# Optimization experiments

Measured on AMD Instinct MI355X. Metric: run time of the kernel, lower is better.

## Reference

```python
import jax, jax.numpy as jnp
import numpy as np

# NF4 codebook (bitsandbytes create_normal_map, quant_type='nf4')
NF4_CODE = jnp.array([
    -1.0, -0.6961928009986877, -0.5250730514526367, -0.39491748809814453,
    -0.28444138169288635, -0.18477343022823334, -0.09105003625154495, 0.0,
    0.07958029955625534, 0.16093020141124725, 0.24611230194568634,
    0.33791524171829224, 0.44070982933044434, 0.5626170039176941,
    0.7229568362236023, 1.0], dtype=jnp.float32)

BLOCKSIZE = 64  # bitsandbytes default
IN_F = 64
OUT_F = 64
N_TOKENS = 1048576


def _quantize_nf4(w_flat):
    # w_flat: [n_blocks, BLOCKSIZE] -> (codes int32, absmax float32)
    absmax = jnp.max(jnp.abs(w_flat), axis=1)  # [n_blocks]
    norm = w_flat / jnp.maximum(absmax, 1e-12)[:, None]
    # nearest NF4 codebook entry
    codes = jnp.argmin(jnp.abs(norm[:, :, None] - NF4_CODE[None, None, :]), axis=-1)
    return codes.astype(jnp.int32), absmax.astype(jnp.float32)


def setup_inputs() -> dict:
    key = jax.random.key(0)
    kx, kw, ka = jax.random.split(key, 3)
    x = jax.random.normal(kx, (N_TOKENS, IN_F), dtype=jnp.float32)
    # frozen base weight, quantized to NF4 blockwise (row-major [out, in] flattened)
    w_base = jax.random.normal(kw, (OUT_F, IN_F), dtype=jnp.float32) * 0.05
    n_blocks = (OUT_F * IN_F) // BLOCKSIZE
    codes, absmax = _quantize_nf4(w_base.reshape(n_blocks, BLOCKSIZE))
    adapter_w = jax.random.normal(ka, (OUT_F, IN_F), dtype=jnp.float32) * 0.05
    return {"x": x, "codes": codes, "absmax": absmax, "adapter_w": adapter_w}


def reference(x, codes, absmax, adapter_w):
    # Blockwise NF4 dequantization of the frozen base weight
    w_base = (NF4_CODE[codes] * absmax[:, None]).reshape(OUT_F, IN_F)  # [out, in]
    # y = x @ W_base^T + x @ A^T  (base(x) + adapter(x))
    return x @ w_base.T + x @ adapter_w.T
```

## Files before the change

kernel.cpp:

```cpp
#include <hip/hip_runtime.h>
#include <hip/hip_bf16.h>


#define N_TOKENS 1048576
#define WROW 36

typedef __attribute__((ext_vector_type(8))) short bf16x8;
typedef __attribute__((ext_vector_type(4))) float f32x4;

__device__ __constant__ float NF4_CODE_D[16] = {
    -1.0f, -0.6961928009986877f, -0.5250730514526367f, -0.39491748809814453f,
    -0.28444138169288635f, -0.18477343022823334f, -0.09105003625154495f, 0.0f,
    0.07958029955625534f, 0.16093020141124725f, 0.24611230194568634f,
    0.33791524171829224f, 0.44070982933044434f, 0.5626170039176941f,
    0.7229568362236023f, 1.0f};

__device__ __forceinline__ unsigned int cvt2(float lo, float hi) {
    __hip_bfloat162 h = __float22bfloat162_rn(make_float2(lo, hi));
    union { __hip_bfloat162 h; unsigned int u; } c; c.h = h;
    return c.u;
}

union BF8 { bf16x8 v; unsigned int u[4]; };

__device__ __forceinline__ void strip_compute(
    f32x4 a0, f32x4 a1, f32x4 a2, f32x4 a3,
    const unsigned int* __restrict__ wbase, float* __restrict__ yp) {
    BF8 b0, b1;
    b0.u[0] = cvt2(a0[0], a0[1]); b0.u[1] = cvt2(a0[2], a0[3]);
    b0.u[2] = cvt2(a1[0], a1[1]); b0.u[3] = cvt2(a1[2], a1[3]);
    b1.u[0] = cvt2(a2[0], a2[1]); b1.u[1] = cvt2(a2[2], a2[3]);
    b1.u[2] = cvt2(a3[0], a3[1]); b1.u[3] = cvt2(a3[2], a3[3]);
#pragma unroll
    for (int j = 0; j < 4; ++j) {
        bf16x8 w0 = *(const bf16x8*)(wbase + j * 16 * WROW);
        bf16x8 w1 = *(const bf16x8*)(wbase + j * 16 * WROW + 16);
        f32x4 c = {0.f, 0.f, 0.f, 0.f};
        c = __builtin_amdgcn_mfma_f32_16x16x32_bf16(w0, b0.v, c, 0, 0, 0);
        c = __builtin_amdgcn_mfma_f32_16x16x32_bf16(w1, b1.v, c, 0, 0, 0);
        __builtin_nontemporal_store(c, (f32x4*)(yp + j * 16));
    }
}

__global__ __launch_bounds__(256) void qlora_fused_kernel(
    const float* __restrict__ x,
    const int* __restrict__ codes,
    const float* __restrict__ absmax,
    const float* __restrict__ adapter,
    float* __restrict__ y) {

    __shared__ unsigned int wlds[64 * WROW];

    const int tid = threadIdx.x;

#pragma unroll
    for (int it = 0; it < 8; ++it) {
        int d = tid + it * 256;
        int r = d >> 5;
        int c = d & 31;
        int e = d * 2;
        float am = absmax[r];
        float w0 = NF4_CODE_D[codes[e]]     * am + adapter[e];
        float w1 = NF4_CODE_D[codes[e + 1]] * am + adapter[e + 1];
        wlds[r * WROW + c] = cvt2(w0, w1);
    }
    __syncthreads();

    const int lane  = tid & 63;
    const int wave  = blockIdx.x * 4 + (tid >> 6);
    const int row16 = lane & 15;
    const int kgrp  = lane >> 4;

    const long base = ((long)wave * 16 + row16) * 64;
    const float* xp = x + base + kgrp * 8;
    float*       yp = y + base + kgrp * 4;
    const long STEP = 8192L * 16 * 64;

    const unsigned int* wbase = &wlds[row16 * WROW + kgrp * 4];

    f32x4 a0 = *(const f32x4*)(xp);
    f32x4 a1 = *(const f32x4*)(xp + 4);
    f32x4 a2 = *(const f32x4*)(xp + 32);
    f32x4 a3 = *(const f32x4*)(xp + 36);

#pragma unroll 1
    for (int i = 0; i < 7; ++i) {
        const float* xn = xp + STEP;
        f32x4 n0 = *(const f32x4*)(xn);
        f32x4 n1 = *(const f32x4*)(xn + 4);
        f32x4 n2 = *(const f32x4*)(xn + 32);
        f32x4 n3 = *(const f32x4*)(xn + 36);

        strip_compute(a0, a1, a2, a3, wbase, yp);

        xp += STEP; yp += STEP;
        a0 = n0; a1 = n1; a2 = n2; a3 = n3;
    }
    strip_compute(a0, a1, a2, a3, wbase, yp);
}

extern "C" void kernel_launch(void* const* d_in, const int* in_sizes, int n_in,
                              void* d_out, int out_size, void* d_ws, size_t ws_size,
                              hipStream_t stream) {
    const float* x       = (const float*)d_in[0];
    const int*   codes   = (const int*)d_in[1];
    const float* absmax  = (const float*)d_in[2];
    const float* adapter = (const float*)d_in[3];
    float* y = (float*)d_out;

    qlora_fused_kernel<<<2048, 256, 0, stream>>>(x, codes, absmax, adapter, y);
}
```

Baseline: 105.1 us.

## Stage MFMA outputs through per-wave LDS to emit coalesced row stores

Each wave now writes its MFMA accumulator tiles into a padded per-wave LDS buffer in two half passes. It then reads them back so that each lane stores contiguous 16-byte chunks of whole output rows, replacing the scattered column-fragment stores. The goal is fully coalesced global writes of y, which is the dominant memory stream. The cost is extra LDS traffic and lgkmcnt waits on every strip. Correctness relies on wave-synchronous execution, with no barrier between the LDS write and read.

```diff
diff --git a/kernel.cpp b/kernel.cpp
--- a/kernel.cpp
+++ b/kernel.cpp
@@ -4,9 +4,12 @@
 
 #define N_TOKENS 1048576
 #define WROW 36
+#define YROW 68
 
 typedef __attribute__((ext_vector_type(8))) short bf16x8;
 typedef __attribute__((ext_vector_type(4))) float f32x4;
+
+#define LDS_XCHG_FENCE() asm volatile("s_waitcnt lgkmcnt(0)" ::: "memory")
 
 __device__ __constant__ float NF4_CODE_D[16] = {
     -1.0f, -0.6961928009986877f, -0.5250730514526367f, -0.39491748809814453f,
@@ -23,25 +26,6 @@
 
 union BF8 { bf16x8 v; unsigned int u[4]; };
 
-__device__ __forceinline__ void strip_compute(
-    f32x4 a0, f32x4 a1, f32x4 a2, f32x4 a3,
-    const unsigned int* __restrict__ wbase, float* __restrict__ yp) {
-    BF8 b0, b1;
-    b0.u[0] = cvt2(a0[0], a0[1]); b0.u[1] = cvt2(a0[2], a0[3]);
-    b0.u[2] = cvt2(a1[0], a1[1]); b0.u[3] = cvt2(a1[2], a1[3]);
-    b1.u[0] = cvt2(a2[0], a2[1]); b1.u[1] = cvt2(a2[2], a2[3]);
-    b1.u[2] = cvt2(a3[0], a3[1]); b1.u[3] = cvt2(a3[2], a3[3]);
-#pragma unroll
-    for (int j = 0; j < 4; ++j) {
-        bf16x8 w0 = *(const bf16x8*)(wbase + j * 16 * WROW);
-        bf16x8 w1 = *(const bf16x8*)(wbase + j * 16 * WROW + 16);
-        f32x4 c = {0.f, 0.f, 0.f, 0.f};
-        c = __builtin_amdgcn_mfma_f32_16x16x32_bf16(w0, b0.v, c, 0, 0, 0);
-        c = __builtin_amdgcn_mfma_f32_16x16x32_bf16(w1, b1.v, c, 0, 0, 0);
-        __builtin_nontemporal_store(c, (f32x4*)(yp + j * 16));
-    }
-}
-
 __global__ __launch_bounds__(256) void qlora_fused_kernel(
     const float* __restrict__ x,
     const int* __restrict__ codes,
@@ -50,6 +34,7 @@
     float* __restrict__ y) {
 
     __shared__ unsigned int wlds[64 * WROW];
+    __shared__ __align__(16) unsigned int ylds[4][8 * YROW];
 
     const int tid = threadIdx.x;
 
@@ -67,16 +52,21 @@
     __syncthreads();
 
     const int lane  = tid & 63;
-    const int wave  = blockIdx.x * 4 + (tid >> 6);
+    const int wv    = tid >> 6;
+    const int wave  = blockIdx.x * 4 + wv;
     const int row16 = lane & 15;
     const int kgrp  = lane >> 4;
 
     const long base = ((long)wave * 16 + row16) * 64;
     const float* xp = x + base + kgrp * 8;
-    float*       yp = y + base + kgrp * 4;
     const long STEP = 8192L * 16 * 64;
 
+    float* yp = y + (long)wave * 1024 + lane * 4;
+
     const unsigned int* wbase = &wlds[row16 * WROW + kgrp * 4];
+    const int mypass = row16 >> 3;
+    unsigned int* ywr = &ylds[wv][(row16 & 7) * YROW + kgrp * 4];
+    const unsigned int* yrd = &ylds[wv][(lane >> 4) * YROW + (lane & 15) * 4];
 
     f32x4 a0 = *(const f32x4*)(xp);
     f32x4 a1 = *(const f32x4*)(xp + 4);
@@ -84,19 +74,50 @@
     f32x4 a3 = *(const f32x4*)(xp + 36);
 
 #pragma unroll 1
-    for (int i = 0; i < 7; ++i) {
-        const float* xn = xp + STEP;
-        f32x4 n0 = *(const f32x4*)(xn);
-        f32x4 n1 = *(const f32x4*)(xn + 4);
-        f32x4 n2 = *(const f32x4*)(xn + 32);
-        f32x4 n3 = *(const f32x4*)(xn + 36);
+    for (int i = 0; i < 8; ++i) {
+        BF8 b0, b1;
+        b0.u[0] = cvt2(a0[0], a0[1]); b0.u[1] = cvt2(a0[2], a0[3]);
+        b0.u[2] = cvt2(a1[0], a1[1]); b0.u[3] = cvt2(a1[2], a1[3]);
+        b1.u[0] = cvt2(a2[0], a2[1]); b1.u[1] = cvt2(a2[2], a2[3]);
+        b1.u[2] = cvt2(a3[0], a3[1]); b1.u[3] = cvt2(a3[2], a3[3]);
 
-        strip_compute(a0, a1, a2, a3, wbase, yp);
+        if (i < 7) {
+            const float* xn = xp + STEP;
+            a0 = *(const f32x4*)(xn);
+            a1 = *(const f32x4*)(xn + 4);
+            a2 = *(const f32x4*)(xn + 32);
+            a3 = *(const f32x4*)(xn + 36);
+            xp += STEP;
+        }
 
-        xp += STEP; yp += STEP;
-        a0 = n0; a1 = n1; a2 = n2; a3 = n3;
+        f32x4 acc[4];
+#pragma unroll
+        for (int j = 0; j < 4; ++j) {
+            bf16x8 w0 = *(const bf16x8*)(wbase + j * 16 * WROW);
+            bf16x8 w1 = *(const bf16x8*)(wbase + j * 16 * WROW + 16);
+            f32x4 c = {0.f, 0.f, 0.f, 0.f};
+            c = __builtin_amdgcn_mfma_f32_16x16x32_bf16(w0, b0.v, c, 0, 0, 0);
+            c = __builtin_amdgcn_mfma_f32_16x16x32_bf16(w1, b1.v, c, 0, 0, 0);
+            acc[j] = c;
+        }
+
+        float* yps = yp + (long)i * STEP;
+#pragma unroll
+        for (int p = 0; p < 2; ++p) {
+            if (mypass == p) {
+#pragma unroll
+                for (int j = 0; j < 4; ++j)
+                    *(f32x4*)(ywr + j * 16) = acc[j];
+            }
+            LDS_XCHG_FENCE();
+#pragma unroll
+            for (int s = 0; s < 2; ++s) {
+                f32x4 v = *(const f32x4*)(yrd + s * 4 * YROW);
+                __builtin_nontemporal_store(v, (f32x4*)(yps + p * 512 + s * 256));
+            }
+            LDS_XCHG_FENCE();
+        }
     }
-    strip_compute(a0, a1, a2, a3, wbase, yp);
 }
 
 extern "C" void kernel_launch(void* const* d_in, const int* in_sizes, int n_in,
```

Result: faster. 85.46 us (-18.7%).
